# Performance work log

Hardware: AMD Instinct MI355X
Metric: run time of the kernel (lower is better)

## Reference

```python
import jax, jax.numpy as jnp
import numpy as np

EMBED = 1024
HEADS = 16
HEAD_DIM = EMBED // HEADS


def setup_inputs() -> dict:
    key = jax.random.key(0)
    k1, k2, k3 = jax.random.split(key, 3)
    hidden_states = jax.random.normal(k1, (2, 2048, EMBED), dtype=jnp.float32)
    # Conv1D weights are stored (nx, nf): y = x @ W + b
    c_attn_w = jax.random.normal(k2, (EMBED, 3 * EMBED), dtype=jnp.float32) * 0.02
    c_attn_b = jnp.zeros((3 * EMBED,), dtype=jnp.float32)
    c_proj_w = jax.random.normal(k3, (EMBED, EMBED), dtype=jnp.float32) * 0.02
    c_proj_b = jnp.zeros((EMBED,), dtype=jnp.float32)
    return {
        "hidden_states": hidden_states,
        "c_attn_w": c_attn_w,
        "c_attn_b": c_attn_b,
        "c_proj_w": c_proj_w,
        "c_proj_b": c_proj_b,
    }


def reference(hidden_states, c_attn_w, c_attn_b, c_proj_w, c_proj_b):
    B, S, E = hidden_states.shape
    H, D = HEADS, HEAD_DIM
    fused = hidden_states @ c_attn_w + c_attn_b  # [B,S,3E]
    q, k, v = jnp.split(fused, 3, axis=-1)
    # split heads -> [B,H,S,D]
    q = q.reshape(B, S, H, D).transpose(0, 2, 1, 3)
    k = k.reshape(B, S, H, D).transpose(0, 2, 1, 3)
    v = v.reshape(B, S, H, D).transpose(0, 2, 1, 3)
    scores = jnp.einsum("bhqd,bhkd->bhqk", q, k) / jnp.sqrt(jnp.float32(D))
    probs = jax.nn.softmax(scores, axis=-1)  # NOTE: no causal mask in source
    attn = jnp.einsum("bhqk,bhkd->bhqd", probs, v)
    out = attn.transpose(0, 2, 1, 3).reshape(B, S, E)
    return out @ c_proj_w + c_proj_b
```

## Files before the change

### kernel.cpp

```cpp
#include <hip/hip_runtime.h>
#include <hip/hip_bf16.h>
#include <cstdint>
#include <cstddef>

#define E_ 1024
#define H_ 16
#define D_ 64
#define B_ 2
#define S_ 2048
#define T_ 4096
#define NQ_ 3072

typedef __bf16 bf16_t;
typedef bf16_t bf16x8 __attribute__((ext_vector_type(8)));
typedef float f32x4 __attribute__((ext_vector_type(4)));

static __device__ __forceinline__ unsigned short f2bf(float f) {
    __hip_bfloat16 h = __float2bfloat16(f);
    return __builtin_bit_cast(unsigned short, h);
}
static __device__ __forceinline__ unsigned pack2(float a, float b) {
    return (unsigned)f2bf(a) | ((unsigned)f2bf(b) << 16);
}
static __device__ __forceinline__ bf16x8 ld_frag(const unsigned short* p) {
    uint4 u = *reinterpret_cast<const uint4*>(p);
    return __builtin_bit_cast(bf16x8, u);
}
static __device__ __forceinline__ void cp16(unsigned short* lds, const unsigned short* g) {
    __builtin_amdgcn_global_load_lds(
        (const __attribute__((address_space(1))) unsigned int*)g,
        (__attribute__((address_space(3))) unsigned int*)lds, 16, 0, 0);
}
static __device__ __forceinline__ f32x4 mfma16(bf16x8 a, bf16x8 b, f32x4 c) {
    return __builtin_amdgcn_mfma_f32_16x16x32_bf16(a, b, c, 0, 0, 0);
}

__global__ __launch_bounds__(256) void k_cvt(const float* __restrict__ in,
                                             unsigned short* __restrict__ out, int n) {
    int i = (blockIdx.x * 256 + threadIdx.x) * 4;
    if (i < n) {
        float4 v = *reinterpret_cast<const float4*>(in + i);
        uint2 o;
        o.x = pack2(v.x, v.y);
        o.y = pack2(v.z, v.w);
        *reinterpret_cast<uint2*>(out + i) = o;
    }
}

__global__ __launch_bounds__(256) void k_wt(const float* __restrict__ in,
                                            unsigned short* __restrict__ out, int K, int N) {
    __shared__ float t[32][33];
    int n0 = blockIdx.x * 32, k0 = blockIdx.y * 32;
    int tx = threadIdx.x, ty = threadIdx.y;
    for (int j = 0; j < 4; j++) {
        int r = ty + j * 8;
        t[r][tx] = in[(size_t)(k0 + r) * N + n0 + tx];
    }
    __syncthreads();
    for (int j = 0; j < 4; j++) {
        int r = ty + j * 8;
        out[(size_t)(n0 + r) * K + k0 + tx] = f2bf(t[tx][r]);
    }
}

static __device__ __forceinline__ void gemm_tile_128(
    const unsigned short* __restrict__ A,
    const unsigned short* __restrict__ Bt,
    int Ktot, int m0, int n0,
    unsigned short* As, unsigned short* Bs,
    f32x4 acc[4][4])
{
    const int t = threadIdx.x;
    const int w = t >> 6, lane = t & 63, lr = lane & 15, lq = lane >> 4;
    const int wm = (w >> 1) * 64, wn = (w & 1) * 64;
    for (int mt = 0; mt < 4; mt++)
        for (int nt = 0; nt < 4; nt++)
            acc[mt][nt] = (f32x4){0.f, 0.f, 0.f, 0.f};

    for (int kt = 0; kt < Ktot; kt += 32) {
        __syncthreads();
        for (int i = 0; i < 2; i++) {
            int c = t + i * 256;
            int row = c >> 2, kp = (c & 3) * 8;
            cp16(&As[c * 8], &A[(size_t)(m0 + row) * Ktot + kt + kp]);
        }
        for (int i = 0; i < 2; i++) {
            int c = t + i * 256;
            int row = c >> 2, kp = (c & 3) * 8;
            cp16(&Bs[c * 8], &Bt[(size_t)(n0 + row) * Ktot + kt + kp]);
        }
        __syncthreads();
        bf16x8 af[4], bfr[4];
        for (int mt = 0; mt < 4; mt++) af[mt]  = ld_frag(&As[(wm + mt * 16 + lr) * 32 + lq * 8]);
        for (int nt = 0; nt < 4; nt++) bfr[nt] = ld_frag(&Bs[(wn + nt * 16 + lr) * 32 + lq * 8]);
        for (int mt = 0; mt < 4; mt++)
            for (int nt = 0; nt < 4; nt++)
                acc[mt][nt] = mfma16(af[mt], bfr[nt], acc[mt][nt]);
    }
}

__global__ __launch_bounds__(256) void k_qkv(
    const unsigned short* __restrict__ Ab, const unsigned short* __restrict__ Wt,
    const float* __restrict__ bias,
    unsigned short* __restrict__ Qb, unsigned short* __restrict__ Kb,
    unsigned short* __restrict__ Vb)
{
    __shared__ __attribute__((aligned(16))) unsigned short As[128 * 32];
    __shared__ __attribute__((aligned(16))) unsigned short Bs[128 * 32];
    f32x4 acc[4][4];
    int m0 = blockIdx.x * 128, n0 = blockIdx.y * 128;
    gemm_tile_128(Ab, Wt, E_, m0, n0, As, Bs, acc);

    int t = threadIdx.x, w = t >> 6, lane = t & 63, lr = lane & 15, lq = lane >> 4;
    int wm = (w >> 1) * 64, wn = (w & 1) * 64;
    int sector = (n0 >> 10);
    for (int nt = 0; nt < 4; nt++) {
        int n = n0 + wn + nt * 16 + lr;
        float bv = bias[n];
        int nn = n & 1023, h = nn >> 6, d = nn & 63;
        for (int mt = 0; mt < 4; mt++) {
            for (int i = 0; i < 4; i++) {
                int tok = m0 + wm + mt * 16 + lq * 4 + i;
                int b = tok >> 11, s = tok & 2047;
                float v = acc[mt][nt][i] + bv;
                if (sector == 0) {
                    Qb[(((size_t)(b * H_ + h) * S_ + s) << 6) + d] = f2bf(v * 0.125f);
                } else if (sector == 1) {
                    Kb[(((size_t)(b * H_ + h) * S_ + s) << 6) + d] = f2bf(v);
                } else {
                    Vb[(((size_t)(b * H_ + h) * D_ + d) << 11) + s] = f2bf(v);
                }
            }
        }
    }
}

__global__ __launch_bounds__(256) void k_attn(
    const unsigned short* __restrict__ Qb, const unsigned short* __restrict__ Kb,
    const unsigned short* __restrict__ Vb, unsigned short* __restrict__ Ob)
{
    __shared__ __attribute__((aligned(16))) unsigned short Ks[128 * 64];
    __shared__ __attribute__((aligned(16))) unsigned short Vt[64 * 128];
    __shared__ __attribute__((aligned(16))) unsigned short Ps[4][16 * 128];

    const int t = threadIdx.x, w = t >> 6, lane = t & 63, lr = lane & 15, lq = lane >> 4;
    const int h = blockIdx.y, b = blockIdx.z;
    const size_t head = ((size_t)(b * H_ + h)) * (S_ * D_);
    const unsigned short* Qh = Qb + head;
    const unsigned short* Kh = Kb + head;
    const unsigned short* Vh = Vb + head;
    const int q0 = blockIdx.x * 64 + w * 16;
    const int swz = lr & 7;

    bf16x8 qa[2];
    for (int kk = 0; kk < 2; kk++)
        qa[kk] = ld_frag(&Qh[(size_t)(q0 + lr) * 64 + kk * 32 + lq * 8]);

    f32x4 o[4];
    for (int i = 0; i < 4; i++) o[i] = (f32x4){0.f, 0.f, 0.f, 0.f};
    float lsum = 0.f;
    unsigned short* Pw = Ps[w];

    for (int kt = 0; kt < S_; kt += 128) {
        __syncthreads();
        for (int i = 0; i < 4; i++) {
            int c = t + i * 256;
            int row = c >> 3, sp = c & 7, seg = sp ^ (row & 7);
            cp16(&Ks[c * 8], &Kh[(size_t)(kt + row) * 64 + seg * 8]);
        }
        for (int i = 0; i < 4; i++) {
            int c = t + i * 256;
            int d = c >> 4, sp = c & 15, seg = (sp & 8) | ((sp & 7) ^ (d & 7));
            cp16(&Vt[c * 8], &Vh[(size_t)d * S_ + kt + seg * 8]);
        }
        __syncthreads();

        float pexp[8][4];
        for (int tau = 0; tau < 8; tau++) {
            f32x4 z = (f32x4){0.f, 0.f, 0.f, 0.f};
            bf16x8 kf0 = ld_frag(&Ks[(tau * 16 + lr) * 64 + ((0 + lq) ^ swz) * 8]);
            bf16x8 kf1 = ld_frag(&Ks[(tau * 16 + lr) * 64 + ((4 + lq) ^ swz) * 8]);
            z = mfma16(kf0, qa[0], z);
            z = mfma16(kf1, qa[1], z);
            for (int r = 0; r < 4; r++) {
                float p = __expf(z[r]);
                pexp[tau][r] = p;
                lsum += p;
            }
        }
        for (int tau = 0; tau < 8; tau++) {
            uint2 pk;
            pk.x = pack2(pexp[tau][0], pexp[tau][1]);
            pk.y = pack2(pexp[tau][2], pexp[tau][3]);
            int seg = (tau * 2 + (lq >> 1)) ^ swz;
            *reinterpret_cast<uint2*>(&Pw[lr * 128 + seg * 8 + (lq & 1) * 4]) = pk;
        }
        for (int kk = 0; kk < 4; kk++) {
            bf16x8 pf = ld_frag(&Pw[lr * 128 + ((kk * 4 + lq) ^ swz) * 8]);
            for (int t2 = 0; t2 < 4; t2++) {
                int seg = kk * 4 + lq;
                int sp = (seg & 8) | ((seg & 7) ^ swz);
                bf16x8 vf = ld_frag(&Vt[(t2 * 16 + lr) * 128 + sp * 8]);
                o[t2] = mfma16(vf, pf, o[t2]);
            }
        }
    }

    lsum += __shfl_xor(lsum, 16, 64);
    lsum += __shfl_xor(lsum, 32, 64);
    float inv = 1.0f / lsum;

    int s = q0 + lr;
    size_t rowoff = ((size_t)(b * S_ + s)) * E_ + h * 64;
    for (int t2 = 0; t2 < 4; t2++) {
        uint2 pk;
        pk.x = pack2(o[t2][0] * inv, o[t2][1] * inv);
        pk.y = pack2(o[t2][2] * inv, o[t2][3] * inv);
        *reinterpret_cast<uint2*>(&Ob[rowoff + t2 * 16 + lq * 4]) = pk;
    }
}

__global__ __launch_bounds__(256) void k_proj(
    const unsigned short* __restrict__ Ab, const unsigned short* __restrict__ Wt,
    const float* __restrict__ bias, float* __restrict__ out)
{
    __shared__ __attribute__((aligned(16))) unsigned short As[128 * 32];
    __shared__ __attribute__((aligned(16))) unsigned short Bs[128 * 32];
    f32x4 acc[4][4];
    int m0 = blockIdx.x * 128, n0 = blockIdx.y * 128;
    gemm_tile_128(Ab, Wt, E_, m0, n0, As, Bs, acc);

    int t = threadIdx.x, w = t >> 6, lane = t & 63, lr = lane & 15, lq = lane >> 4;
    int wm = (w >> 1) * 64, wn = (w & 1) * 64;
    for (int nt = 0; nt < 4; nt++) {
        int n = n0 + wn + nt * 16 + lr;
        float bv = bias[n];
        for (int mt = 0; mt < 4; mt++)
            for (int i = 0; i < 4; i++) {
                int tok = m0 + wm + mt * 16 + lq * 4 + i;
                out[(size_t)tok * E_ + n] = acc[mt][nt][i] + bv;
            }
    }
}

extern "C" void kernel_launch(void* const* d_in, const int* in_sizes, int n_in,
                              void* d_out, int out_size, void* d_ws, size_t ws_size,
                              hipStream_t stream) {
    const float* hs = (const float*)d_in[0];
    const float* w1 = (const float*)d_in[1];
    const float* b1 = (const float*)d_in[2];
    const float* w2 = (const float*)d_in[3];
    const float* b2 = (const float*)d_in[4];
    float* out = (float*)d_out;

    char* ws = (char*)d_ws;
    unsigned short* hb  = (unsigned short*)(ws);
    unsigned short* w1t = (unsigned short*)(ws + (size_t)( 8 << 20));
    unsigned short* w2t = (unsigned short*)(ws + (size_t)(14 << 20));
    unsigned short* Qb  = (unsigned short*)(ws + (size_t)(16 << 20));
    unsigned short* Kb  = (unsigned short*)(ws + (size_t)(24 << 20));
    unsigned short* Vb  = (unsigned short*)(ws + (size_t)(32 << 20));
    unsigned short* Ao  = (unsigned short*)(ws + (size_t)(40 << 20));

    k_cvt<<<dim3(T_ * E_ / 1024), dim3(256), 0, stream>>>(hs, hb, T_ * E_);
    k_wt<<<dim3(NQ_ / 32, E_ / 32), dim3(32, 8), 0, stream>>>(w1, w1t, E_, NQ_);
    k_wt<<<dim3(E_ / 32, E_ / 32), dim3(32, 8), 0, stream>>>(w2, w2t, E_, E_);
    k_qkv<<<dim3(T_ / 128, NQ_ / 128), dim3(256), 0, stream>>>(hb, w1t, b1, Qb, Kb, Vb);
    k_attn<<<dim3(S_ / 64, H_, B_), dim3(256), 0, stream>>>(Qb, Kb, Vb, Ao);
    k_proj<<<dim3(T_ / 128, E_ / 128), dim3(256), 0, stream>>>(Ao, w2t, b2, out);
}
```

Measured before the change: 217.4 us.

## Split attention key tiles across waves and store GEMM tiles in fragment order

In the attention kernel, each wave now covers all 64 queries of the block but only a quarter of each 128-key tile. The waves' partial outputs and row sums are then reduced through shared memory before normalizing and writing. K and V tiles are stored in shared memory in MFMA fragment order, so each lane loads its fragment contiguously without swizzling. The same fragment-ordered layout is applied to the GEMM A/B tiles. This cuts redundant LDS fragment reads, since Q is held in registers and each K/V fragment is read by one wave. The cost is more accumulator registers (16 output tiles per wave) and a serialized cross-wave reduction at the end.

```diff
diff --git a/kernel.cpp b/kernel.cpp
--- a/kernel.cpp
+++ b/kernel.cpp
@@ -71,8 +71,8 @@
     f32x4 acc[4][4])
 {
     const int t = threadIdx.x;
-    const int w = t >> 6, lane = t & 63, lr = lane & 15, lq = lane >> 4;
-    const int wm = (w >> 1) * 64, wn = (w & 1) * 64;
+    const int w = t >> 6, lane = t & 63;
+    const int wmg = (w >> 1) * 4, wng = (w & 1) * 4;
     for (int mt = 0; mt < 4; mt++)
         for (int nt = 0; nt < 4; nt++)
             acc[mt][nt] = (f32x4){0.f, 0.f, 0.f, 0.f};
@@ -81,18 +81,18 @@
         __syncthreads();
         for (int i = 0; i < 2; i++) {
             int c = t + i * 256;
-            int row = c >> 2, kp = (c & 3) * 8;
-            cp16(&As[c * 8], &A[(size_t)(m0 + row) * Ktot + kt + kp]);
+            int rg = c >> 6, kc = (c >> 4) & 3, r = c & 15;
+            cp16(&As[c * 8], &A[(size_t)(m0 + rg * 16 + r) * Ktot + kt + kc * 8]);
         }
         for (int i = 0; i < 2; i++) {
             int c = t + i * 256;
-            int row = c >> 2, kp = (c & 3) * 8;
-            cp16(&Bs[c * 8], &Bt[(size_t)(n0 + row) * Ktot + kt + kp]);
+            int rg = c >> 6, kc = (c >> 4) & 3, r = c & 15;
+            cp16(&Bs[c * 8], &Bt[(size_t)(n0 + rg * 16 + r) * Ktot + kt + kc * 8]);
         }
         __syncthreads();
         bf16x8 af[4], bfr[4];
-        for (int mt = 0; mt < 4; mt++) af[mt]  = ld_frag(&As[(wm + mt * 16 + lr) * 32 + lq * 8]);
-        for (int nt = 0; nt < 4; nt++) bfr[nt] = ld_frag(&Bs[(wn + nt * 16 + lr) * 32 + lq * 8]);
+        for (int mt = 0; mt < 4; mt++) af[mt]  = ld_frag(&As[((wmg + mt) * 64 + lane) * 8]);
+        for (int nt = 0; nt < 4; nt++) bfr[nt] = ld_frag(&Bs[((wng + nt) * 64 + lane) * 8]);
         for (int mt = 0; mt < 4; mt++)
             for (int nt = 0; nt < 4; nt++)
                 acc[mt][nt] = mfma16(af[mt], bfr[nt], acc[mt][nt]);
@@ -139,84 +139,120 @@
     const unsigned short* __restrict__ Qb, const unsigned short* __restrict__ Kb,
     const unsigned short* __restrict__ Vb, unsigned short* __restrict__ Ob)
 {
-    __shared__ __attribute__((aligned(16))) unsigned short Ks[128 * 64];
-    __shared__ __attribute__((aligned(16))) unsigned short Vt[64 * 128];
-    __shared__ __attribute__((aligned(16))) unsigned short Ps[4][16 * 128];
+    __shared__ __attribute__((aligned(16))) unsigned short smem[25088];
+    unsigned short* Ks = smem;
+    unsigned short* Vt = smem + 8192;
+    float* Lred = (float*)(smem + 24576);
+    float* Ored = (float*)smem;
 
     const int t = threadIdx.x, w = t >> 6, lane = t & 63, lr = lane & 15, lq = lane >> 4;
+    unsigned short* Pw = smem + 16384 + w * 2048;
+
     const int h = blockIdx.y, b = blockIdx.z;
     const size_t head = ((size_t)(b * H_ + h)) * (S_ * D_);
     const unsigned short* Qh = Qb + head;
     const unsigned short* Kh = Kb + head;
     const unsigned short* Vh = Vb + head;
-    const int q0 = blockIdx.x * 64 + w * 16;
-    const int swz = lr & 7;
-
-    bf16x8 qa[2];
-    for (int kk = 0; kk < 2; kk++)
-        qa[kk] = ld_frag(&Qh[(size_t)(q0 + lr) * 64 + kk * 32 + lq * 8]);
-
-    f32x4 o[4];
-    for (int i = 0; i < 4; i++) o[i] = (f32x4){0.f, 0.f, 0.f, 0.f};
-    float lsum = 0.f;
-    unsigned short* Pw = Ps[w];
+    const int q0 = blockIdx.x * 64;
+
+    bf16x8 qf[4][2];
+    for (int qt = 0; qt < 4; qt++)
+        for (int dc = 0; dc < 2; dc++)
+            qf[qt][dc] = ld_frag(&Qh[(size_t)(q0 + qt * 16 + lr) * 64 + dc * 32 + lq * 8]);
+
+    f32x4 o[4][4];
+    for (int qt = 0; qt < 4; qt++)
+        for (int dt = 0; dt < 4; dt++)
+            o[qt][dt] = (f32x4){0.f, 0.f, 0.f, 0.f};
+    float lsum[4] = {0.f, 0.f, 0.f, 0.f};
 
     for (int kt = 0; kt < S_; kt += 128) {
         __syncthreads();
         for (int i = 0; i < 4; i++) {
-            int c = t + i * 256;
-            int row = c >> 3, sp = c & 7, seg = sp ^ (row & 7);
-            cp16(&Ks[c * 8], &Kh[(size_t)(kt + row) * 64 + seg * 8]);
+            int p = t + i * 256;
+            int g = p >> 6, lq_ = (p >> 4) & 3, lr_ = p & 15;
+            int ktile = g >> 1, dc = g & 1;
+            cp16(&Ks[p * 8], &Kh[(size_t)(kt + ktile * 16 + lr_) * 64 + dc * 32 + lq_ * 8]);
         }
         for (int i = 0; i < 4; i++) {
-            int c = t + i * 256;
-            int d = c >> 4, sp = c & 15, seg = (sp & 8) | ((sp & 7) ^ (d & 7));
-            cp16(&Vt[c * 8], &Vh[(size_t)d * S_ + kt + seg * 8]);
-        }
-        __syncthreads();
-
-        float pexp[8][4];
-        for (int tau = 0; tau < 8; tau++) {
-            f32x4 z = (f32x4){0.f, 0.f, 0.f, 0.f};
-            bf16x8 kf0 = ld_frag(&Ks[(tau * 16 + lr) * 64 + ((0 + lq) ^ swz) * 8]);
-            bf16x8 kf1 = ld_frag(&Ks[(tau * 16 + lr) * 64 + ((4 + lq) ^ swz) * 8]);
-            z = mfma16(kf0, qa[0], z);
-            z = mfma16(kf1, qa[1], z);
-            for (int r = 0; r < 4; r++) {
-                float p = __expf(z[r]);
-                pexp[tau][r] = p;
-                lsum += p;
+            int p = t + i * 256;
+            int g = p >> 6, lq_ = (p >> 4) & 3, lr_ = p & 15;
+            int wv = g >> 2, dt = g & 3;
+            cp16(&Vt[p * 8], &Vh[(size_t)(dt * 16 + lr_) * S_ + kt + wv * 32 + lq_ * 8]);
+        }
+        __syncthreads();
+
+        f32x4 z[2][4];
+        for (int ktl = 0; ktl < 2; ktl++) {
+            int kt2 = (w * 2 + ktl) * 2;
+            bf16x8 kf0 = ld_frag(&Ks[((kt2 + 0) * 64 + lane) * 8]);
+            bf16x8 kf1 = ld_frag(&Ks[((kt2 + 1) * 64 + lane) * 8]);
+            for (int qt = 0; qt < 4; qt++) {
+                f32x4 zz = (f32x4){0.f, 0.f, 0.f, 0.f};
+                zz = mfma16(kf0, qf[qt][0], zz);
+                zz = mfma16(kf1, qf[qt][1], zz);
+                z[ktl][qt] = zz;
             }
         }
-        for (int tau = 0; tau < 8; tau++) {
-            uint2 pk;
-            pk.x = pack2(pexp[tau][0], pexp[tau][1]);
-            pk.y = pack2(pexp[tau][2], pexp[tau][3]);
-            int seg = (tau * 2 + (lq >> 1)) ^ swz;
-            *reinterpret_cast<uint2*>(&Pw[lr * 128 + seg * 8 + (lq & 1) * 4]) = pk;
-        }
-        for (int kk = 0; kk < 4; kk++) {
-            bf16x8 pf = ld_frag(&Pw[lr * 128 + ((kk * 4 + lq) ^ swz) * 8]);
-            for (int t2 = 0; t2 < 4; t2++) {
-                int seg = kk * 4 + lq;
-                int sp = (seg & 8) | ((seg & 7) ^ swz);
-                bf16x8 vf = ld_frag(&Vt[(t2 * 16 + lr) * 128 + sp * 8]);
-                o[t2] = mfma16(vf, pf, o[t2]);
+        for (int ktl = 0; ktl < 2; ktl++) {
+            for (int qt = 0; qt < 4; qt++) {
+                float p0 = __expf(z[ktl][qt][0]);
+                float p1 = __expf(z[ktl][qt][1]);
+                float p2 = __expf(z[ktl][qt][2]);
+                float p3 = __expf(z[ktl][qt][3]);
+                lsum[qt] += (p0 + p1) + (p2 + p3);
+                uint2 pk;
+                pk.x = pack2(p0, p1);
+                pk.y = pack2(p2, p3);
+                *reinterpret_cast<uint2*>(
+                    &Pw[(qt * 64 + (ktl * 2 + (lq >> 1)) * 16 + lr) * 8 + (lq & 1) * 4]) = pk;
             }
         }
-    }
-
-    lsum += __shfl_xor(lsum, 16, 64);
-    lsum += __shfl_xor(lsum, 32, 64);
-    float inv = 1.0f / lsum;
-
-    int s = q0 + lr;
-    size_t rowoff = ((size_t)(b * S_ + s)) * E_ + h * 64;
-    for (int t2 = 0; t2 < 4; t2++) {
-        uint2 pk;
-        pk.x = pack2(o[t2][0] * inv, o[t2][1] * inv);
-        pk.y = pack2(o[t2][2] * inv, o[t2][3] * inv);
-        *reinterpret_cast<uint2*>(&Ob[rowoff + t2 * 16 + lq * 4]) = pk;
+        bf16x8 vf[4];
+        for (int dt = 0; dt < 4; dt++)
+            vf[dt] = ld_frag(&Vt[((w * 4 + dt) * 64 + lane) * 8]);
+        for (int qt = 0; qt < 4; qt++) {
+            bf16x8 pf = ld_frag(&Pw[(qt * 64 + lane) * 8]);
+            for (int dt = 0; dt < 4; dt++)
+                o[qt][dt] = mfma16(pf, vf[dt], o[qt][dt]);
+        }
+    }
+
+    __syncthreads();
+
+    for (int qt = 0; qt < 4; qt++) {
+        lsum[qt] += __shfl_xor(lsum[qt], 16, 64);
+        lsum[qt] += __shfl_xor(lsum[qt], 32, 64);
+    }
+    if (lq == 0)
+        for (int qt = 0; qt < 4; qt++)
+            Lred[w * 64 + qt * 16 + lr] = lsum[qt];
+
+    for (int ww = 0; ww < 4; ww++) {
+        if (w == ww) {
+            for (int qt = 0; qt < 4; qt++)
+                for (int dt = 0; dt < 4; dt++)
+                    for (int r = 0; r < 4; r++) {
+                        int q = qt * 16 + lq * 4 + r, d = dt * 16 + lr;
+                        if (ww == 0) Ored[q * 68 + d] = o[qt][dt][r];
+                        else         Ored[q * 68 + d] += o[qt][dt][r];
+                    }
+        }
+        __syncthreads();
+    }
+
+    {
+        int q = t >> 2, dsg = (t & 3) * 16;
+        float inv = 1.0f / (Lred[q] + Lred[64 + q] + Lred[128 + q] + Lred[192 + q]);
+        const float* rp = &Ored[q * 68 + dsg];
+        unsigned u[8];
+        for (int j = 0; j < 8; j++)
+            u[j] = pack2(rp[2 * j] * inv, rp[2 * j + 1] * inv);
+        size_t off = ((size_t)(b * S_ + q0 + q)) * E_ + h * 64 + dsg;
+        uint4 s0 = {u[0], u[1], u[2], u[3]};
+        uint4 s1 = {u[4], u[5], u[6], u[7]};
+        *reinterpret_cast<uint4*>(&Ob[off]) = s0;
+        *reinterpret_cast<uint4*>(&Ob[off + 8]) = s1;
     }
 }
 
```

Result: slower. 257.8 us (+18.6%).
